# Kernel optimization log

Measured on AMD Instinct MI355X. Metric: run time of the kernel, lower is better.

The kernel has to match this reference:

```python
import jax, jax.numpy as jnp
import numpy as np

BLOCK = 64  # quantization block size along in_features
IN, OUT, RANK, ALPHA = 4096, 4096, 16, 32
SCALING = ALPHA / RANK


def setup_inputs() -> dict:
    key = jax.random.key(0)
    ks = jax.random.split(key, 6)
    x = jax.random.normal(ks[0], (8, 1024, IN), dtype=jnp.float32)
    # int4 codes in [0, 15]; dequant subtracts 8 -> [-8, 7]
    qweight = jax.random.randint(ks[1], (OUT, IN), 0, 16, dtype=jnp.int32)
    # blockwise absmax-style scales, small positive
    scales = jax.random.uniform(ks[2], (OUT, IN // BLOCK), dtype=jnp.float32) * 0.02 + 1e-3
    bias = jax.random.normal(ks[3], (OUT,), dtype=jnp.float32) * 0.02
    lora_A = jax.random.normal(ks[4], (IN, RANK), dtype=jnp.float32) * 0.02
    lora_B = jnp.zeros((RANK, OUT), dtype=jnp.float32)
    return {"x": x, "qweight": qweight, "scales": scales, "bias": bias,
            "lora_A": lora_A, "lora_B": lora_B}


def _dequant(qweight, scales):
    # qweight: [out, in] int codes in [0,15]; scales: [out, in/BLOCK]
    out, in_f = qweight.shape
    q = (qweight.astype(jnp.float32) - 8.0).reshape(out, in_f // BLOCK, BLOCK)
    return (q * scales[:, :, None]).reshape(out, in_f)  # [out, in]


def reference(x, qweight, scales, bias, lora_A, lora_B):
    W = _dequant(qweight, scales)                      # [out, in]
    base = jnp.einsum('bsi,oi->bso', x, W) + bias      # quantized linear
    lora = jnp.einsum('bsr,ro->bso', jnp.einsum('bsi,ir->bsr', x, lora_A), lora_B)
    return base + lora * SCALING
```

## Files before the change

### kernel.cpp

```cpp
#include <hip/hip_runtime.h>
#include <hip/hip_bf16.h>

#define IN_F 4096
#define OUT_F 4096
#define M_TOK 8192
#define RANK 16

typedef __attribute__((ext_vector_type(4))) float f32x4;
typedef __attribute__((ext_vector_type(8))) short short8;

struct alignas(16) bf16x8_s { __hip_bfloat16 v[8]; };

#define DEQ_BLOCKS 2048

__global__ __launch_bounds__(256) void deq_kernel(
    const int* __restrict__ q,
    const float* __restrict__ scales,
    const float* __restrict__ lA,
    const float* __restrict__ lB,
    __hip_bfloat16* __restrict__ W) {
    const int tid = threadIdx.x;
    const int bid = blockIdx.x;
    const int o0 = (bid >> 1) * 4;
    const int i0 = (bid & 1) * 2048 + tid * 8;

    float bw[16][4];
#pragma unroll
    for (int r = 0; r < 16; ++r)
#pragma unroll
        for (int oi = 0; oi < 4; ++oi)
            bw[r][oi] = 2.0f * lB[(size_t)r * OUT_F + o0 + oi];

    float fold[4][8];
#pragma unroll
    for (int e = 0; e < 8; ++e) {
        const float* ar = lA + (size_t)(i0 + e) * RANK;
        float4 a0 = *(const float4*)(ar + 0);
        float4 a1 = *(const float4*)(ar + 4);
        float4 a2 = *(const float4*)(ar + 8);
        float4 a3 = *(const float4*)(ar + 12);
#pragma unroll
        for (int oi = 0; oi < 4; ++oi) {
            float f = a0.x * bw[0][oi] + a0.y * bw[1][oi]
                    + a0.z * bw[2][oi] + a0.w * bw[3][oi]
                    + a1.x * bw[4][oi] + a1.y * bw[5][oi]
                    + a1.z * bw[6][oi] + a1.w * bw[7][oi]
                    + a2.x * bw[8][oi] + a2.y * bw[9][oi]
                    + a2.z * bw[10][oi] + a2.w * bw[11][oi]
                    + a3.x * bw[12][oi] + a3.y * bw[13][oi]
                    + a3.z * bw[14][oi] + a3.w * bw[15][oi];
            fold[oi][e] = f;
        }
    }

#pragma unroll
    for (int oi = 0; oi < 4; ++oi) {
        const int o = o0 + oi;
        const float s = scales[o * 64 + (i0 >> 6)];
        const int4* qp = (const int4*)(q + (size_t)o * IN_F + i0);
        int4 q0 = qp[0];
        int4 q1 = qp[1];
        bf16x8_s r;
        r.v[0] = __float2bfloat16(s * (float)(q0.x - 8) + fold[oi][0]);
        r.v[1] = __float2bfloat16(s * (float)(q0.y - 8) + fold[oi][1]);
        r.v[2] = __float2bfloat16(s * (float)(q0.z - 8) + fold[oi][2]);
        r.v[3] = __float2bfloat16(s * (float)(q0.w - 8) + fold[oi][3]);
        r.v[4] = __float2bfloat16(s * (float)(q1.x - 8) + fold[oi][4]);
        r.v[5] = __float2bfloat16(s * (float)(q1.y - 8) + fold[oi][5]);
        r.v[6] = __float2bfloat16(s * (float)(q1.z - 8) + fold[oi][6]);
        r.v[7] = __float2bfloat16(s * (float)(q1.w - 8) + fold[oi][7]);
        *(bf16x8_s*)(W + (size_t)o * IN_F + i0) = r;
    }
}

#define BK 64
#define NT (IN_F / BK)

__device__ __forceinline__ short8 ldfrag(const short* p, int half, int row, int gran) {
    return *(const short8*)(p + half * 8192 + row * 64 + ((gran ^ (row & 7)) * 8));
}

#define STAGE_B(LDSbuf, ROW0, K0)                                             \
    {                                                                         \
        _Pragma("unroll")                                                     \
        for (int j = 0; j < 2; ++j) {                                         \
            const __hip_bfloat16* g = Wq +                                    \
                (size_t)((ROW0) + j * 64 + wave * 8 + srow) * IN_F + (K0) + sgc; \
            __builtin_amdgcn_global_load_lds(                                 \
                (const __attribute__((address_space(1))) void*)g,             \
                (__attribute__((address_space(3))) void*)((LDSbuf) + (j * 64 + wave * 8) * 64), \
                16, 0, 0);                                                    \
        }                                                                     \
    }

#define LOAD_A_F32(K0)                                                        \
    {                                                                         \
        _Pragma("unroll")                                                     \
        for (int h = 0; h < 2; ++h)                                           \
        _Pragma("unroll")                                                     \
        for (int j = 0; j < 2; ++j) {                                         \
            const float* gp = xf +                                            \
                (size_t)(m0 + h * 128 + j * 64 + wave * 8 + srow) * IN_F +    \
                (K0) + (lane & 7) * 8;                                        \
            axf[h * 2 + j][0] = *(const float4*)gp;                           \
            axf[h * 2 + j][1] = *(const float4*)(gp + 4);                     \
        }                                                                     \
    }

#define WRITE_A(DSTBUF, H)                                                    \
    {                                                                         \
        _Pragma("unroll")                                                     \
        for (int j = 0; j < 2; ++j) {                                         \
            bf16x8_s pk;                                                      \
            const float4 u0 = axf[(H) * 2 + j][0];                            \
            const float4 u1 = axf[(H) * 2 + j][1];                            \
            pk.v[0] = __float2bfloat16(u0.x); pk.v[1] = __float2bfloat16(u0.y); \
            pk.v[2] = __float2bfloat16(u0.z); pk.v[3] = __float2bfloat16(u0.w); \
            pk.v[4] = __float2bfloat16(u1.x); pk.v[5] = __float2bfloat16(u1.y); \
            pk.v[6] = __float2bfloat16(u1.z); pk.v[7] = __float2bfloat16(u1.w); \
            __hip_bfloat16* dst = (DSTBUF) + (H) * 8192 +                     \
                (j * 64 + wave * 8 + srow) * 64 + ((lane & 7) ^ srow) * 8;    \
            *(bf16x8_s*)dst = pk;                                             \
        }                                                                     \
    }

#define RD_A(BUF, HALF, KG)                                                   \
    _Pragma("unroll") for (int f = 0; f < 4; ++f)                             \
        fa[f] = ldfrag(BUF, HALF, wm * 64 + f * 16 + fr, (KG) * 4 + fc);

#define RD_B(BUF, KG)                                                         \
    _Pragma("unroll") for (int g2 = 0; g2 < 4; ++g2)                          \
        fb[g2] = ldfrag(BUF, bhalf, brow0 + g2 * 16 + fr, (KG) * 4 + fc);

#define MFMA16(MH)                                                            \
    _Pragma("unroll") for (int f = 0; f < 4; ++f)                             \
    _Pragma("unroll") for (int g2 = 0; g2 < 4; ++g2)                          \
        acc[(MH) * 4 + f][g2] = __builtin_amdgcn_mfma_f32_16x16x32_bf16(      \
            fa[f], fb[g2], acc[(MH) * 4 + f][g2], 0, 0, 0);

#define BAR __builtin_amdgcn_s_barrier();

__global__ __launch_bounds__(512, 2) void qlora_gemm_kernel(
    const float* __restrict__ xf,
    const __hip_bfloat16* __restrict__ Wq,
    const float* __restrict__ bias,
    float* __restrict__ out) {
    __shared__ __hip_bfloat16 As[2][16384];
    __shared__ __hip_bfloat16 Bs[2][16384];

    const int tid  = threadIdx.x;
    const int wave = tid >> 6;
    const int lane = tid & 63;
    const int wm = wave >> 2;
    const int wn = wave & 3;

    const int wg = ((int)blockIdx.x & 7) * 32 + ((int)blockIdx.x >> 3);
    const int bx = wg & 15;
    const int by = wg >> 4;
    const int m0 = by * 256;
    const int n0 = bx * 256;

    f32x4 acc[8][4];
#pragma unroll
    for (int i = 0; i < 8; ++i)
#pragma unroll
        for (int j = 0; j < 4; ++j)
            acc[i][j] = (f32x4){0.f, 0.f, 0.f, 0.f};

    const int srow = lane >> 3;
    const int sgc  = ((lane & 7) ^ srow) * 8;

    const int fr = lane & 15;
    const int fc = lane >> 4;

    const int bhalf = wn >> 1;
    const int brow0 = (wn & 1) * 64;

    const short* A0p = (const short*)As[0];
    const short* A1p = (const short*)As[1];
    const short* B0p = (const short*)Bs[0];
    const short* B1p = (const short*)Bs[1];

    short8 fa[4];
    short8 fb[4];
    float4 axf[4][2];

    LOAD_A_F32(0);
    STAGE_B(Bs[0],        n0,       0);
    STAGE_B(Bs[0] + 8192, n0 + 128, 0);
    STAGE_B(Bs[1],        n0,       BK);
    WRITE_A(As[0], 0);
    WRITE_A(As[0], 1);
    asm volatile("s_waitcnt lgkmcnt(0)" ::: "memory");
    asm volatile("s_waitcnt vmcnt(2)" ::: "memory");

    for (int it = 0; it < NT / 2; ++it) {
        const int t = it * 2;
        const int k_t1 = (t + 1) * BK;
        const int k_t2 = ((t + 2) & (NT - 1)) * BK;
        const int k_t3 = ((t + 3) & (NT - 1)) * BK;

        BAR RD_A(A0p, 0, 0) RD_B(B0p, 0)
            LOAD_A_F32(k_t1)
            MFMA16(0)
        BAR RD_A(A0p, 1, 0)
            STAGE_B(Bs[1] + 8192, n0 + 128, k_t1)
            MFMA16(1)
        BAR RD_A(A0p, 0, 1) RD_B(B0p, 1)
            WRITE_A((__hip_bfloat16*)As[1], 0)
            MFMA16(0)
        BAR RD_A(A0p, 1, 1)
            STAGE_B(Bs[0], n0, k_t2)
            WRITE_A((__hip_bfloat16*)As[1], 1)
            MFMA16(1)
        asm volatile("s_waitcnt lgkmcnt(0)" ::: "memory");
        asm volatile("s_waitcnt vmcnt(2)" ::: "memory");

        BAR RD_A(A1p, 0, 0) RD_B(B1p, 0)
            LOAD_A_F32(k_t2)
            MFMA16(0)
        BAR RD_A(A1p, 1, 0)
            STAGE_B(Bs[0] + 8192, n0 + 128, k_t2)
            MFMA16(1)
        BAR RD_A(A1p, 0, 1) RD_B(B1p, 1)
            WRITE_A((__hip_bfloat16*)As[0], 0)
            MFMA16(0)
        BAR RD_A(A1p, 1, 1)
            STAGE_B(Bs[1], n0, k_t3)
            WRITE_A((__hip_bfloat16*)As[0], 1)
            MFMA16(1)
        asm volatile("s_waitcnt lgkmcnt(0)" ::: "memory");
        asm volatile("s_waitcnt vmcnt(2)" ::: "memory");
    }

    asm volatile("s_waitcnt vmcnt(0)" ::: "memory");

    const int cc  = lane & 15;
    const int rr4 = (lane >> 4) * 4;
    float bv[4];
#pragma unroll
    for (int g2 = 0; g2 < 4; ++g2)
        bv[g2] = bias[n0 + wn * 64 + g2 * 16 + cc];

#pragma unroll
    for (int mh = 0; mh < 2; ++mh)
#pragma unroll
        for (int f = 0; f < 4; ++f) {
            const int m = m0 + mh * 128 + wm * 64 + f * 16 + rr4;
#pragma unroll
            for (int g2 = 0; g2 < 4; ++g2) {
                const int n = n0 + wn * 64 + g2 * 16 + cc;
                float* op = out + (size_t)m * OUT_F + n;
                const f32x4 a = acc[mh * 4 + f][g2];
#pragma unroll
                for (int r = 0; r < 4; ++r)
                    op[(size_t)r * OUT_F] = a[r] + bv[g2];
            }
        }
}

extern "C" void kernel_launch(void* const* d_in, const int* in_sizes, int n_in,
                              void* d_out, int out_size, void* d_ws, size_t ws_size,
                              hipStream_t stream) {
    const float* x      = (const float*)d_in[0];
    const int*   qw     = (const int*)  d_in[1];
    const float* scales = (const float*)d_in[2];
    const float* bias   = (const float*)d_in[3];
    const float* lA     = (const float*)d_in[4];
    const float* lB     = (const float*)d_in[5];
    float* out = (float*)d_out;

    __hip_bfloat16* Wq = (__hip_bfloat16*)d_ws;

    deq_kernel<<<DEQ_BLOCKS, 256, 0, stream>>>(qw, scales, lA, lB, Wq);
    const size_t xhalf = (size_t)4096 * IN_F;
    const size_t ohalf = (size_t)4096 * OUT_F;
    qlora_gemm_kernel<<<dim3(256), dim3(512), 0, stream>>>(x, Wq, bias, out);
    qlora_gemm_kernel<<<dim3(256), dim3(512), 0, stream>>>(x + xhalf, Wq, bias, out + ohalf);
}
```

Baseline: 663.4 us.

## Double-buffer fp32 activation registers to prefetch A two tiles ahead

Splits the fp32 activation staging registers into even and odd sets so global loads of x are issued two K-tiles ahead instead of one. The B staging is reordered to come first, and the vmcnt waits are relaxed so the in-flight A loads are not waited on early. The aim is to hide more global-load latency of the fp32 activations behind MFMA work. The cost is doubled staging registers, which may lower occupancy or cause spills, and the hand-counted vmcnt value must match the actual number of outstanding loads to stay correct.

```diff
diff --git a/kernel.cpp b/kernel.cpp
--- a/kernel.cpp
+++ b/kernel.cpp
@@ -80,6 +80,8 @@
     return *(const short8*)(p + half * 8192 + row * 64 + ((gran ^ (row & 7)) * 8));
 }
 
+#define FENCE asm volatile("" ::: "memory");
+
 #define STAGE_B(LDSbuf, ROW0, K0)                                             \
     {                                                                         \
         _Pragma("unroll")                                                     \
@@ -93,7 +95,7 @@
         }                                                                     \
     }
 
-#define LOAD_A_F32(K0)                                                        \
+#define LOAD_A_F32(SET, K0)                                                   \
     {                                                                         \
         _Pragma("unroll")                                                     \
         for (int h = 0; h < 2; ++h)                                           \
@@ -102,18 +104,18 @@
             const float* gp = xf +                                            \
                 (size_t)(m0 + h * 128 + j * 64 + wave * 8 + srow) * IN_F +    \
                 (K0) + (lane & 7) * 8;                                        \
-            axf[h * 2 + j][0] = *(const float4*)gp;                           \
-            axf[h * 2 + j][1] = *(const float4*)(gp + 4);                     \
+            SET[h * 2 + j][0] = *(const float4*)gp;                           \
+            SET[h * 2 + j][1] = *(const float4*)(gp + 4);                     \
         }                                                                     \
     }
 
-#define WRITE_A(DSTBUF, H)                                                    \
+#define WRITE_A(SET, DSTBUF, H)                                               \
     {                                                                         \
         _Pragma("unroll")                                                     \
         for (int j = 0; j < 2; ++j) {                                         \
             bf16x8_s pk;                                                      \
-            const float4 u0 = axf[(H) * 2 + j][0];                            \
-            const float4 u1 = axf[(H) * 2 + j][1];                            \
+            const float4 u0 = SET[(H) * 2 + j][0];                            \
+            const float4 u1 = SET[(H) * 2 + j][1];                            \
             pk.v[0] = __float2bfloat16(u0.x); pk.v[1] = __float2bfloat16(u0.y); \
             pk.v[2] = __float2bfloat16(u0.z); pk.v[3] = __float2bfloat16(u0.w); \
             pk.v[4] = __float2bfloat16(u1.x); pk.v[5] = __float2bfloat16(u1.y); \
@@ -183,16 +185,21 @@
 
     short8 fa[4];
     short8 fb[4];
-    float4 axf[4][2];
-
-    LOAD_A_F32(0);
+    float4 axfE[4][2];
+    float4 axfO[4][2];
+
+    LOAD_A_F32(axfE, 0);
+    FENCE
     STAGE_B(Bs[0],        n0,       0);
     STAGE_B(Bs[0] + 8192, n0 + 128, 0);
-    STAGE_B(Bs[1],        n0,       BK);
-    WRITE_A(As[0], 0);
-    WRITE_A(As[0], 1);
+    WRITE_A(axfE, (__hip_bfloat16*)As[0], 0);
+    WRITE_A(axfE, (__hip_bfloat16*)As[0], 1);
+    FENCE
+    LOAD_A_F32(axfO, BK);
+    FENCE
+    STAGE_B(Bs[1], n0, BK);
     asm volatile("s_waitcnt lgkmcnt(0)" ::: "memory");
-    asm volatile("s_waitcnt vmcnt(2)" ::: "memory");
+    asm volatile("s_waitcnt vmcnt(10)" ::: "memory");
 
     for (int it = 0; it < NT / 2; ++it) {
         const int t = it * 2;
@@ -201,36 +208,38 @@
         const int k_t3 = ((t + 3) & (NT - 1)) * BK;
 
         BAR RD_A(A0p, 0, 0) RD_B(B0p, 0)
-            LOAD_A_F32(k_t1)
+            STAGE_B(Bs[1] + 8192, n0 + 128, k_t1)
+            FENCE
+            LOAD_A_F32(axfE, k_t2)
             MFMA16(0)
         BAR RD_A(A0p, 1, 0)
-            STAGE_B(Bs[1] + 8192, n0 + 128, k_t1)
             MFMA16(1)
         BAR RD_A(A0p, 0, 1) RD_B(B0p, 1)
-            WRITE_A((__hip_bfloat16*)As[1], 0)
+            WRITE_A(axfO, (__hip_bfloat16*)As[1], 0)
             MFMA16(0)
         BAR RD_A(A0p, 1, 1)
             STAGE_B(Bs[0], n0, k_t2)
-            WRITE_A((__hip_bfloat16*)As[1], 1)
+            WRITE_A(axfO, (__hip_bfloat16*)As[1], 1)
             MFMA16(1)
         asm volatile("s_waitcnt lgkmcnt(0)" ::: "memory");
-        asm volatile("s_waitcnt vmcnt(2)" ::: "memory");
+        asm volatile("s_waitcnt vmcnt(10)" ::: "memory");
 
         BAR RD_A(A1p, 0, 0) RD_B(B1p, 0)
-            LOAD_A_F32(k_t2)
+            STAGE_B(Bs[0] + 8192, n0 + 128, k_t2)
+            FENCE
+            LOAD_A_F32(axfO, k_t3)
             MFMA16(0)
         BAR RD_A(A1p, 1, 0)
-            STAGE_B(Bs[0] + 8192, n0 + 128, k_t2)
             MFMA16(1)
         BAR RD_A(A1p, 0, 1) RD_B(B1p, 1)
-            WRITE_A((__hip_bfloat16*)As[0], 0)
+            WRITE_A(axfE, (__hip_bfloat16*)As[0], 0)
             MFMA16(0)
         BAR RD_A(A1p, 1, 1)
             STAGE_B(Bs[1], n0, k_t3)
-            WRITE_A((__hip_bfloat16*)As[0], 1)
+            WRITE_A(axfE, (__hip_bfloat16*)As[0], 1)
             MFMA16(1)
         asm volatile("s_waitcnt lgkmcnt(0)" ::: "memory");
-        asm volatile("s_waitcnt vmcnt(2)" ::: "memory");
+        asm volatile("s_waitcnt vmcnt(10)" ::: "memory");
     }
 
     asm volatile("s_waitcnt vmcnt(0)" ::: "memory");
```

New measurement: 893.1 us. 1.35x slower.
